# Performance work log

Hardware: AMD Instinct MI355X
Metric: run time of the kernel (lower is better)

Reference implementation:

```python
import jax, jax.numpy as jnp
import numpy as np

B, T, C = 4, 2048, 768
H, D = 6, 128


def apply_rotary_emb(x, cos, sin):
    # x: (B, T, H, D); cos, sin: (1, T, 1, D//2)
    d = x.shape[-1] // 2
    x1, x2 = x[..., :d], x[..., d:]
    y1 = x1 * cos + x2 * sin
    y2 = -x1 * sin + x2 * cos
    return jnp.concatenate([y1, y2], axis=-1)


def rmsnorm(x):
    eps = 1e-15
    ms = jnp.mean(x * x, axis=-1, keepdims=True)
    return x / jnp.sqrt(ms + eps)


def setup_inputs() -> dict:
    key = jax.random.key(0)
    ks = jax.random.split(key, 7)
    s = 0.02
    return {
        "x": jax.random.normal(ks[0], (B, T, C), jnp.float32),
        "cos": jax.random.normal(ks[1], (1, T, 1, D // 2), jnp.float32),
        "sin": jax.random.normal(ks[2], (1, T, 1, D // 2), jnp.float32),
        "Wq": jax.random.normal(ks[3], (C, C), jnp.float32) * s,
        "Wk": jax.random.normal(ks[4], (C, C), jnp.float32) * s,
        "Wv": jax.random.normal(ks[5], (C, C), jnp.float32) * s,
        "Wo": jax.random.normal(ks[6], (C, C), jnp.float32) * s,
    }


def reference(x, cos, sin, Wq, Wk, Wv, Wo):
    b, t, c = x.shape
    # QKV projections (nn.Linear: x @ W.T)
    q = (x @ Wq.T).reshape(b, t, H, D)
    k = (x @ Wk.T).reshape(b, t, H, D)
    v = (x @ Wv.T).reshape(b, t, H, D)
    # RoPE then QK-RMSNorm
    q = rmsnorm(apply_rotary_emb(q, cos, sin))
    k = rmsnorm(apply_rotary_emb(k, cos, sin))
    # (B, H, T, D)
    q = q.transpose(0, 2, 1, 3)
    k = k.transpose(0, 2, 1, 3)
    v = v.transpose(0, 2, 1, 3)
    scores = jnp.einsum('bhqd,bhkd->bhqk', q, k) / jnp.sqrt(jnp.float32(D))
    causal = jnp.tril(jnp.ones((t, t), dtype=bool))
    scores = jnp.where(causal[None, None], scores, -jnp.inf)
    attn = jax.nn.softmax(scores, axis=-1)
    out = jnp.einsum('bhqk,bhkd->bhqd', attn, v)
    out = out.transpose(0, 2, 1, 3).reshape(b, t, c)
    return out @ Wo.T
```

## Files before the change

### kernel.cpp

```cpp
#include <hip/hip_runtime.h>

#define T_SEQ 2048
#define NH    6
#define HD    128
#define CDIM  768
#define NQKV  2304
#define MROWS 8192
#define NSLOT 1104
#define QSCL  0.12754011021989615f

typedef __attribute__((ext_vector_type(8)))  short bf16x8;
typedef __attribute__((ext_vector_type(4)))  float f32x4;
typedef __attribute__((ext_vector_type(16))) float f32x16;
typedef __attribute__((ext_vector_type(2)))  int   i32x2;

__device__ __forceinline__ unsigned short f2bf(float f){
  unsigned int u = __builtin_bit_cast(unsigned int, f);
  u += 0x7fffu + ((u >> 16) & 1u);
  return (unsigned short)(u >> 16);
}
__device__ __forceinline__ float bf2f(unsigned short h){
  unsigned int u = ((unsigned int)h) << 16;
  return __builtin_bit_cast(float, u);
}
__device__ __forceinline__ float ex2(float x){
  return __builtin_amdgcn_exp2f(x);
}
__device__ __forceinline__ unsigned int cvtpk(float lo, float hi){
  unsigned int r;
  asm("v_cvt_pk_bf16_f32 %0, %1, %2" : "=v"(r) : "v"(lo), "v"(hi));
  return r;
}

__device__ __forceinline__ void gload_lds16(const void* g, void* l){
  __builtin_amdgcn_global_load_lds(
      (const __attribute__((address_space(1))) unsigned int*)g,
      (__attribute__((address_space(3))) unsigned int*)l, 16, 0, 0);
}

__device__ __forceinline__ int ncq(int Q){
  return Q < 3 ? 1 : Q < 7 ? 2 : Q < 10 ? 3 : Q < 14 ? 4 : 5;
}
__device__ __forceinline__ int cumc(int Q){
  return Q < 4 ? Q : Q < 8 ? 3 + 2*(Q-3) : Q < 11 ? 11 + 3*(Q-7)
       : Q < 15 ? 20 + 4*(Q-10) : 36 + 5*(Q-14);
}

__global__ __launch_bounds__(256) void cvt_f32_bf16(
    const float* __restrict__ in, unsigned short* __restrict__ out, int n4){
  int i = blockIdx.x * 256 + threadIdx.x;
  if (i >= n4) return;
  float4 v = reinterpret_cast<const float4*>(in)[i];
  ushort4 o;
  o.x = f2bf(v.x); o.y = f2bf(v.y); o.z = f2bf(v.z); o.w = f2bf(v.w);
  reinterpret_cast<ushort4*>(out)[i] = o;
}

__global__ __launch_bounds__(256) void cvt_w4(
    const float* __restrict__ w0, const float* __restrict__ w1,
    const float* __restrict__ w2, const float* __restrict__ w3,
    unsigned short* __restrict__ out){
  const int which = blockIdx.y;
  const float* src = which == 0 ? w0 : which == 1 ? w1 : which == 2 ? w2 : w3;
  int i = blockIdx.x * 256 + threadIdx.x;
  float4 v = reinterpret_cast<const float4*>(src)[i];
  ushort4 o;
  o.x = f2bf(v.x); o.y = f2bf(v.y); o.z = f2bf(v.z); o.w = f2bf(v.w);
  reinterpret_cast<ushort4*>(out + (size_t)which * CDIM * CDIM)[i] = o;
}

template<int EPI>
__global__ __launch_bounds__(256) void gemm_bt(
    const unsigned short* __restrict__ A,
    const unsigned short* __restrict__ B,
    void* __restrict__ Cv, int M, int N, int K,
    const float* __restrict__ cosp, const float* __restrict__ sinp,
    unsigned short* __restrict__ Vt)
{
  __shared__ unsigned short sh[128 * 128];
  unsigned short* As = sh;
  unsigned short* Bs = sh + 128 * 64;
  const int tid  = threadIdx.x;
  const int lane = tid & 63;
  const int wave = tid >> 6;
  const int lr = lane & 15, lg = lane >> 4;
  const int srow = lane >> 3;
  const int sslot = (lane & 7) ^ (lane >> 3);
  const int gx = gridDim.x, gy = gridDim.y, nwg = gx * gy;
  const int flat = blockIdx.y * gx + blockIdx.x;
  const int nf = (flat & 7) * (nwg >> 3) + (flat >> 3);
  const int row0 = (nf / gy) * 128, col0 = (nf % gy) * 128;
  const int wrow = wave * 32;

  f32x4 acc[2][8];
  const f32x4 z = {0.f, 0.f, 0.f, 0.f};
  #pragma unroll
  for (int i = 0; i < 2; ++i)
    #pragma unroll
    for (int j = 0; j < 8; ++j) acc[i][j] = z;

  for (int k0 = 0; k0 < K; k0 += 64){
    #pragma unroll
    for (int i = 0; i < 4; ++i){
      int seg = wave * 4 + i;
      int r = seg * 8 + srow;
      gload_lds16(&A[(size_t)(row0 + r) * K + k0 + sslot * 8], &As[seg * 512]);
      gload_lds16(&B[(size_t)(col0 + r) * K + k0 + sslot * 8], &Bs[seg * 512]);
    }
    __syncthreads();
    #pragma unroll
    for (int kk = 0; kk < 64; kk += 32){
      bf16x8 af[2], bfr[8];
      #pragma unroll
      for (int mi = 0; mi < 2; ++mi)
        af[mi] = *reinterpret_cast<const bf16x8*>(
            &As[(wrow + mi*16 + lr) * 64 + ((((kk>>3) + lg) ^ (lr & 7)) * 8)]);
      #pragma unroll
      for (int ni = 0; ni < 8; ++ni)
        bfr[ni] = *reinterpret_cast<const bf16x8*>(
            &Bs[(ni*16 + lr) * 64 + ((((kk>>3) + lg) ^ (lr & 7)) * 8)]);
      #pragma unroll
      for (int mi = 0; mi < 2; ++mi)
        #pragma unroll
        for (int ni = 0; ni < 8; ++ni)
          acc[mi][ni] = __builtin_amdgcn_mfma_f32_16x16x32_bf16(af[mi], bfr[ni], acc[mi][ni], 0, 0, 0);
    }
    __syncthreads();
  }

  if (EPI == 0){
    float* Cf = reinterpret_cast<float*>(Cv);
    #pragma unroll
    for (int mi = 0; mi < 2; ++mi)
      #pragma unroll
      for (int ni = 0; ni < 8; ++ni)
        #pragma unroll
        for (int r = 0; r < 4; ++r)
          Cf[(size_t)(row0 + wrow + mi*16 + lg*4 + r) * N + col0 + ni*16 + lr] = acc[mi][ni][r];
  } else {
    unsigned short* Cb = reinterpret_cast<unsigned short*>(Cv);
    const int ct = col0 >> 7;
    if (ct >= 12){
      const int hh = ct - 12;
      const int b2 = row0 >> 11, t0 = row0 & (T_SEQ - 1);
      #pragma unroll
      for (int mi = 0; mi < 2; ++mi)
        #pragma unroll
        for (int ni = 0; ni < 8; ++ni)
          #pragma unroll
          for (int r = 0; r < 4; ++r){
            const int trow = wrow + mi*16 + lg*4 + r;
            const int col  = ni*16 + lr;
            sh[trow * 128 + (col ^ ((trow & 7) << 4))] = f2bf(acc[mi][ni][r]);
          }
      __syncthreads();
      const int dd = tid >> 1, tq = (tid & 1) * 64;
      unsigned short* dst =
          Vt + ((size_t)(b2 * NH + hh) * HD + dd) * T_SEQ + t0 + tq;
      #pragma unroll
      for (int j8 = 0; j8 < 8; ++j8){
        union { int4 v; unsigned short u[8]; } w;
        #pragma unroll
        for (int jj = 0; jj < 8; ++jj){
          const int tt = tq + j8 * 8 + jj;
          w.u[jj] = sh[tt * 128 + (dd ^ (jj << 4))];
        }
        *reinterpret_cast<int4*>(&dst[j8 * 8]) = w.v;
      }
    } else {
      const float post = (ct < 6) ? QSCL : 1.0f;
      #pragma unroll
      for (int mi = 0; mi < 2; ++mi){
        #pragma unroll
        for (int r = 0; r < 4; ++r){
          const int row = row0 + wrow + mi*16 + lg*4 + r;
          const int t = row & (T_SEQ - 1);
          float y1[4], y2[4], ssp = 0.f;
          #pragma unroll
          for (int ni = 0; ni < 4; ++ni){
            const int d = ni*16 + lr;
            float c = cosp[t * 64 + d];
            float s = sinp[t * 64 + d];
            float x1 = acc[mi][ni][r], x2 = acc[mi][ni+4][r];
            y1[ni] = x1 * c + x2 * s;
            y2[ni] = x2 * c - x1 * s;
            ssp += y1[ni]*y1[ni] + y2[ni]*y2[ni];
          }
          #pragma unroll
          for (int off = 1; off < 16; off <<= 1) ssp += __shfl_xor(ssp, off);
          const float inv = rsqrtf(ssp * (1.0f / 128.0f) + 1e-15f) * post;
          #pragma unroll
          for (int ni = 0; ni < 4; ++ni){
            const int d = ni*16 + lr;
            Cb[(size_t)row * N + col0 + d]      = f2bf(y1[ni] * inv);
            Cb[(size_t)row * N + col0 + d + 64] = f2bf(y2[ni] * inv);
          }
        }
      }
    }
  }
}

__global__ __launch_bounds__(256) void attn_fwd(
    const unsigned short* __restrict__ QKVb,
    const unsigned short* __restrict__ Vt,
    unsigned short* __restrict__ AO,
    unsigned short* __restrict__ Op, float* __restrict__ Mp, float* __restrict__ Lp)
{
  __shared__ unsigned short Ks[64][136];
  __shared__ unsigned short Vs[128][72];
  const int tid = threadIdx.x;
  const int lane = tid & 63, wave = tid >> 6;
  const int l31 = lane & 31, hi = lane >> 5;

  const int flat = blockIdx.x;
  const int nf = (flat & 7) * 138 + (flat >> 3);
  const int bh = nf / 46;
  const int L = 45 - (nf % 46);
  int Q, c;
  if (L < 3)      { Q = L; c = 0; }
  else if (L < 11){ int m = L - 3;  Q = 3 + (m >> 1);  c = m & 1; }
  else if (L < 20){ int m = L - 11; Q = 7 + m / 3;     c = m % 3; }
  else if (L < 36){ int m = L - 20; Q = 10 + (m >> 2); c = m & 3; }
  else            { int m = L - 36; Q = 14 + m / 5;    c = m % 5; }
  const int nc = ncq(Q);
  const int tiles = 2 * Q + 2;
  const int base = tiles / nc, rem = tiles % nc;
  const int tbeg = c * base + (c < rem ? c : rem);
  const int tend = tbeg + base + (c < rem ? 1 : 0);
  const int b = bh / NH, h = bh % NH;
  const int qw = Q * 128 + wave * 32;

  const unsigned short* Qp = QKVb + (size_t)(b * T_SEQ) * NQKV + h * HD;
  const unsigned short* Kp = QKVb + (size_t)(b * T_SEQ) * NQKV + CDIM + h * HD;
  const unsigned short* Vp = Vt + (size_t)bh * HD * T_SEQ;

  const int kr = tid >> 4, kc4 = (tid & 15) * 8;
  const int vr = tid >> 3, vc4 = (tid & 7) * 8;

  bf16x8 qf[8];
  #pragma unroll
  for (int c4 = 0; c4 < 8; ++c4)
    qf[c4] = *reinterpret_cast<const bf16x8*>(
        &Qp[(size_t)(qw + l31) * NQKV + c4 * 16 + hi * 8]);

  f32x16 o[4];
  #pragma unroll
  for (int db = 0; db < 4; ++db)
    #pragma unroll
    for (int r = 0; r < 16; ++r) o[db][r] = 0.f;
  float mrun = -__builtin_inff(), lrun = 0.f;

  int4 gk0, gk1, gk2, gk3, gv0, gv1, gv2, gv3;
  {
    const int kv0 = tbeg * 64;
    gk0 = *reinterpret_cast<const int4*>(&Kp[(size_t)(kv0 + kr)       * NQKV + kc4]);
    gk1 = *reinterpret_cast<const int4*>(&Kp[(size_t)(kv0 + kr + 16)  * NQKV + kc4]);
    gk2 = *reinterpret_cast<const int4*>(&Kp[(size_t)(kv0 + kr + 32)  * NQKV + kc4]);
    gk3 = *reinterpret_cast<const int4*>(&Kp[(size_t)(kv0 + kr + 48)  * NQKV + kc4]);
    gv0 = *reinterpret_cast<const int4*>(&Vp[(size_t)(vr)       * T_SEQ + kv0 + vc4]);
    gv1 = *reinterpret_cast<const int4*>(&Vp[(size_t)(vr + 32)  * T_SEQ + kv0 + vc4]);
    gv2 = *reinterpret_cast<const int4*>(&Vp[(size_t)(vr + 64)  * T_SEQ + kv0 + vc4]);
    gv3 = *reinterpret_cast<const int4*>(&Vp[(size_t)(vr + 96)  * T_SEQ + kv0 + vc4]);
  }

  for (int t = tbeg; t < tend; ++t){
    *reinterpret_cast<int4*>(&Ks[kr][kc4])        = gk0;
    *reinterpret_cast<int4*>(&Ks[kr + 16][kc4])   = gk1;
    *reinterpret_cast<int4*>(&Ks[kr + 32][kc4])   = gk2;
    *reinterpret_cast<int4*>(&Ks[kr + 48][kc4])   = gk3;
    *reinterpret_cast<int4*>(&Vs[vr][vc4])        = gv0;
    *reinterpret_cast<int4*>(&Vs[vr + 32][vc4])   = gv1;
    *reinterpret_cast<int4*>(&Vs[vr + 64][vc4])   = gv2;
    *reinterpret_cast<int4*>(&Vs[vr + 96][vc4])   = gv3;
    __syncthreads();

    if (t + 1 < tend){
      const int kn = (t + 1) * 64;
      gk0 = *reinterpret_cast<const int4*>(&Kp[(size_t)(kn + kr)       * NQKV + kc4]);
      gk1 = *reinterpret_cast<const int4*>(&Kp[(size_t)(kn + kr + 16)  * NQKV + kc4]);
      gk2 = *reinterpret_cast<const int4*>(&Kp[(size_t)(kn + kr + 32)  * NQKV + kc4]);
      gk3 = *reinterpret_cast<const int4*>(&Kp[(size_t)(kn + kr + 48)  * NQKV + kc4]);
      gv0 = *reinterpret_cast<const int4*>(&Vp[(size_t)(vr)       * T_SEQ + kn + vc4]);
      gv1 = *reinterpret_cast<const int4*>(&Vp[(size_t)(vr + 32)  * T_SEQ + kn + vc4]);
      gv2 = *reinterpret_cast<const int4*>(&Vp[(size_t)(vr + 64)  * T_SEQ + kn + vc4]);
      gv3 = *reinterpret_cast<const int4*>(&Vp[(size_t)(vr + 96)  * T_SEQ + kn + vc4]);
    }

    const int kv0 = t * 64;
    if (kv0 <= qw + 31){
      f32x16 s[2];
      #pragma unroll
      for (int r = 0; r < 16; ++r){ s[0][r] = 0.f; s[1][r] = 0.f; }
      __builtin_amdgcn_s_setprio(1);
      #pragma unroll
      for (int c4 = 0; c4 < 8; ++c4){
        bf16x8 k0 = *reinterpret_cast<const bf16x8*>(&Ks[l31][c4 * 16 + hi * 8]);
        bf16x8 k1 = *reinterpret_cast<const bf16x8*>(&Ks[32 + l31][c4 * 16 + hi * 8]);
        s[0] = __builtin_amdgcn_mfma_f32_32x32x16_bf16(k0, qf[c4], s[0], 0, 0, 0);
        s[1] = __builtin_amdgcn_mfma_f32_32x32x16_bf16(k1, qf[c4], s[1], 0, 0, 0);
      }
      __builtin_amdgcn_s_setprio(0);

      const int qg = qw + l31;
      if (kv0 + 63 > qw){
        #pragma unroll
        for (int blk = 0; blk < 2; ++blk)
          #pragma unroll
          for (int r = 0; r < 16; ++r){
            int kg = kv0 + 32 * blk + (r & 3) + 8 * (r >> 2) + 4 * hi;
            s[blk][r] = (kg <= qg) ? s[blk][r] : -__builtin_inff();
          }
      }

      float t8[8];
      #pragma unroll
      for (int blk = 0; blk < 2; ++blk)
        #pragma unroll
        for (int j = 0; j < 4; ++j)
          t8[blk * 4 + j] = fmaxf(fmaxf(s[blk][4*j], s[blk][4*j+1]),
                                  fmaxf(s[blk][4*j+2], s[blk][4*j+3]));
      float pm = fmaxf(fmaxf(fmaxf(t8[0], t8[1]), fmaxf(t8[2], t8[3])),
                       fmaxf(fmaxf(t8[4], t8[5]), fmaxf(t8[6], t8[7])));
      pm = fmaxf(pm, __shfl_xor(pm, 32));

      if (__any(pm > mrun)){
        float mn = fmaxf(mrun, pm);
        float scf = (mrun == -__builtin_inff()) ? 0.f : ex2(mrun - mn);
        mrun = mn; lrun *= scf;
        #pragma unroll
        for (int r = 0; r < 16; ++r){
          float scr = __shfl(scf, (r & 3) + 8 * (r >> 2) + 4 * hi, 32);
          #pragma unroll
          for (int db = 0; db < 4; ++db) o[db][r] *= scr;
        }
      }

      float a8[8];
      #pragma unroll
      for (int blk = 0; blk < 2; ++blk)
        #pragma unroll
        for (int j = 0; j < 4; ++j){
          float p0 = ex2(s[blk][4*j]   - mrun);
          float p1 = ex2(s[blk][4*j+1] - mrun);
          float p2 = ex2(s[blk][4*j+2] - mrun);
          float p3 = ex2(s[blk][4*j+3] - mrun);
          s[blk][4*j] = p0; s[blk][4*j+1] = p1; s[blk][4*j+2] = p2; s[blk][4*j+3] = p3;
          a8[blk * 4 + j] = (p0 + p1) + (p2 + p3);
        }
      float ls = ((a8[0] + a8[1]) + (a8[2] + a8[3])) + ((a8[4] + a8[5]) + (a8[6] + a8[7]));
      lrun += ls + __shfl_xor(ls, 32);

      __builtin_amdgcn_s_setprio(1);
      #pragma unroll
      for (int kc = 0; kc < 4; ++kc){
        const int blk = kc >> 1, base2 = (kc & 1) * 8;
        unsigned int a0 = cvtpk(s[blk][base2+0], s[blk][base2+1]);
        unsigned int b0 = cvtpk(s[blk][base2+4], s[blk][base2+5]);
        unsigned int a1 = cvtpk(s[blk][base2+2], s[blk][base2+3]);
        unsigned int b1 = cvtpk(s[blk][base2+6], s[blk][base2+7]);
        i32x2 sw0 = __builtin_amdgcn_permlane32_swap((int)a0, (int)b0, false, false);
        i32x2 sw1 = __builtin_amdgcn_permlane32_swap((int)a1, (int)b1, false, false);
        union { bf16x8 v; unsigned int u[4]; } pa;
        pa.u[0] = (unsigned int)sw0[0];
        pa.u[1] = (unsigned int)sw1[0];
        pa.u[2] = (unsigned int)sw0[1];
        pa.u[3] = (unsigned int)sw1[1];
        #pragma unroll
        for (int db = 0; db < 4; ++db){
          bf16x8 vf = *reinterpret_cast<const bf16x8*>(
              &Vs[db * 32 + l31][kc * 16 + hi * 8]);
          o[db] = __builtin_amdgcn_mfma_f32_32x32x16_bf16(pa.v, vf, o[db], 0, 0, 0);
        }
      }
      __builtin_amdgcn_s_setprio(0);
    }
    __syncthreads();
  }

  if (nc == 1){
    float inv = 1.0f / lrun;
    #pragma unroll
    for (int r = 0; r < 16; ++r){
      const int crow = (r & 3) + 8 * (r >> 2) + 4 * hi;
      float ir = __shfl(inv, crow, 32);
      #pragma unroll
      for (int db = 0; db < 4; ++db)
        AO[((size_t)b * T_SEQ + qw + crow) * CDIM + h * HD + db * 32 + l31] =
            f2bf(o[db][r] * ir);
    }
  } else {
    const int slot = bh * 46 + cumc(Q) + c;
    unsigned short* OpW = Op + (size_t)slot * 128 * 128;
    #pragma unroll
    for (int r = 0; r < 16; ++r){
      const int row = wave * 32 + (r & 3) + 8 * (r >> 2) + 4 * hi;
      #pragma unroll
      for (int db = 0; db < 4; ++db)
        OpW[row * 128 + db * 32 + l31] = f2bf(o[db][r]);
    }
    if (hi == 0){
      Mp[(size_t)slot * 128 + wave * 32 + l31] = mrun;
      Lp[(size_t)slot * 128 + wave * 32 + l31] = lrun;
    }
  }
}

__global__ __launch_bounds__(256) void attn_combine(
    const unsigned short* __restrict__ Op, const float* __restrict__ Mp,
    const float* __restrict__ Lp, unsigned short* __restrict__ AO)
{
  const int Q  = 3 + blockIdx.x;
  const int bh = blockIdx.y;
  const int b = bh / NH, h = bh % NH;
  const int nc = ncq(Q);
  const int slot0 = bh * 46 + cumc(Q);
  #pragma unroll
  for (int u = 0; u < 16; ++u){
    int unit = threadIdx.x + u * 256;
    int r = unit >> 5, d4 = unit & 31;
    float m = -__builtin_inff();
    for (int cc = 0; cc < nc; ++cc)
      m = fmaxf(m, Mp[(size_t)(slot0 + cc) * 128 + r]);
    float l = 0.f;
    float a0 = 0.f, a1 = 0.f, a2 = 0.f, a3 = 0.f;
    for (int cc = 0; cc < nc; ++cc){
      float w = __builtin_amdgcn_exp2f(Mp[(size_t)(slot0 + cc) * 128 + r] - m);
      l += w * Lp[(size_t)(slot0 + cc) * 128 + r];
      const ushort4 v = *reinterpret_cast<const ushort4*>(
          &Op[((size_t)(slot0 + cc) * 128 + r) * 128 + d4 * 4]);
      a0 += w * bf2f(v.x); a1 += w * bf2f(v.y);
      a2 += w * bf2f(v.z); a3 += w * bf2f(v.w);
    }
    float inv = 1.0f / l;
    ushort4 ov;
    ov.x = f2bf(a0 * inv); ov.y = f2bf(a1 * inv);
    ov.z = f2bf(a2 * inv); ov.w = f2bf(a3 * inv);
    *reinterpret_cast<ushort4*>(
        &AO[((size_t)b * T_SEQ + Q * 128 + r) * CDIM + h * HD + d4 * 4]) = ov;
  }
}

extern "C" void kernel_launch(void* const* d_in, const int* in_sizes, int n_in,
                              void* d_out, int out_size, void* d_ws, size_t ws_size,
                              hipStream_t stream)
{
  (void)in_sizes; (void)n_in; (void)out_size; (void)ws_size;
  const float* x    = (const float*)d_in[0];
  const float* cosp = (const float*)d_in[1];
  const float* sinp = (const float*)d_in[2];
  const float* Wq   = (const float*)d_in[3];
  const float* Wk   = (const float*)d_in[4];
  const float* Wv   = (const float*)d_in[5];
  const float* Wo   = (const float*)d_in[6];
  float* out = (float*)d_out;

  unsigned short* xb    = (unsigned short*)d_ws;
  unsigned short* Wqkvb = xb    + (size_t)MROWS * CDIM;
  unsigned short* Wob   = Wqkvb + (size_t)NQKV * CDIM;
  unsigned short* QKVb  = Wob   + (size_t)CDIM * CDIM;
  unsigned short* Vtb   = QKVb  + (size_t)MROWS * NQKV;
  unsigned short* AO    = Vtb   + (size_t)MROWS * CDIM;
  unsigned short* Op    = AO    + (size_t)MROWS * CDIM;
  float* Mp = (float*)(Op + (size_t)NSLOT * 128 * 128);
  float* Lp = Mp + (size_t)NSLOT * 128;

  int n4x = MROWS * CDIM / 4;
  cvt_f32_bf16<<<(n4x + 255) / 256, 256, 0, stream>>>(x, xb, n4x);
  cvt_w4<<<dim3(CDIM * CDIM / 4 / 256, 4), 256, 0, stream>>>(Wq, Wk, Wv, Wo, Wqkvb);

  gemm_bt<1><<<dim3(MROWS / 128, NQKV / 128), 256, 0, stream>>>(
      xb, Wqkvb, QKVb, MROWS, NQKV, CDIM, cosp, sinp, Vtb);
  attn_fwd<<<NSLOT, 256, 0, stream>>>(QKVb, Vtb, AO, Op, Mp, Lp);
  attn_combine<<<dim3(13, 24), 256, 0, stream>>>(Op, Mp, Lp, AO);
  gemm_bt<0><<<dim3(MROWS / 128, CDIM / 128), 256, 0, stream>>>(
      AO, Wob, out, MROWS, CDIM, CDIM, nullptr, nullptr, nullptr);
}
```

Baseline: 210.2 us.

## Load K/V tiles directly to LDS with XOR swizzle instead of register staging

Replaces the register-staged K/V prefetch (global loads held in registers across the loop, then written to padded LDS) with direct global-to-LDS 16-byte loads (gload_lds16) into unpadded, XOR-swizzled LDS layouts. Fragment reads apply the same swizzle to avoid bank conflicts, and launch bounds request 4 blocks per SM. This removes the register pressure and LDS write instructions of the staging path, but also drops the software prefetch overlap, so each tile's load latency is now exposed before the barrier unless occupancy hides it.

```diff
diff --git a/kernel.cpp b/kernel.cpp
--- a/kernel.cpp
+++ b/kernel.cpp
@@ -201,14 +201,14 @@
   }
 }
 
-__global__ __launch_bounds__(256) void attn_fwd(
+__global__ __launch_bounds__(256, 4) void attn_fwd(
     const unsigned short* __restrict__ QKVb,
     const unsigned short* __restrict__ Vt,
     unsigned short* __restrict__ AO,
     unsigned short* __restrict__ Op, float* __restrict__ Mp, float* __restrict__ Lp)
 {
-  __shared__ unsigned short Ks[64][136];
-  __shared__ unsigned short Vs[128][72];
+  __shared__ unsigned short Ks[64 * 128];
+  __shared__ unsigned short Vs[128 * 64];
   const int tid = threadIdx.x;
   const int lane = tid & 63, wave = tid >> 6;
   const int l31 = lane & 31, hi = lane >> 5;
@@ -235,8 +235,10 @@
   const unsigned short* Kp = QKVb + (size_t)(b * T_SEQ) * NQKV + CDIM + h * HD;
   const unsigned short* Vp = Vt + (size_t)bh * HD * T_SEQ;
 
-  const int kr = tid >> 4, kc4 = (tid & 15) * 8;
-  const int vr = tid >> 3, vc4 = (tid & 7) * 8;
+  const int krow_in = lane >> 4;
+  const int kslot   = lane & 15;
+  const int vrow_in = lane >> 3;
+  const int vslot   = lane & 7;
 
   bf16x8 qf[8];
   #pragma unroll
@@ -251,43 +253,21 @@
     for (int r = 0; r < 16; ++r) o[db][r] = 0.f;
   float mrun = -__builtin_inff(), lrun = 0.f;
 
-  int4 gk0, gk1, gk2, gk3, gv0, gv1, gv2, gv3;
-  {
-    const int kv0 = tbeg * 64;
-    gk0 = *reinterpret_cast<const int4*>(&Kp[(size_t)(kv0 + kr)       * NQKV + kc4]);
-    gk1 = *reinterpret_cast<const int4*>(&Kp[(size_t)(kv0 + kr + 16)  * NQKV + kc4]);
-    gk2 = *reinterpret_cast<const int4*>(&Kp[(size_t)(kv0 + kr + 32)  * NQKV + kc4]);
-    gk3 = *reinterpret_cast<const int4*>(&Kp[(size_t)(kv0 + kr + 48)  * NQKV + kc4]);
-    gv0 = *reinterpret_cast<const int4*>(&Vp[(size_t)(vr)       * T_SEQ + kv0 + vc4]);
-    gv1 = *reinterpret_cast<const int4*>(&Vp[(size_t)(vr + 32)  * T_SEQ + kv0 + vc4]);
-    gv2 = *reinterpret_cast<const int4*>(&Vp[(size_t)(vr + 64)  * T_SEQ + kv0 + vc4]);
-    gv3 = *reinterpret_cast<const int4*>(&Vp[(size_t)(vr + 96)  * T_SEQ + kv0 + vc4]);
-  }
-
   for (int t = tbeg; t < tend; ++t){
-    *reinterpret_cast<int4*>(&Ks[kr][kc4])        = gk0;
-    *reinterpret_cast<int4*>(&Ks[kr + 16][kc4])   = gk1;
-    *reinterpret_cast<int4*>(&Ks[kr + 32][kc4])   = gk2;
-    *reinterpret_cast<int4*>(&Ks[kr + 48][kc4])   = gk3;
-    *reinterpret_cast<int4*>(&Vs[vr][vc4])        = gv0;
-    *reinterpret_cast<int4*>(&Vs[vr + 32][vc4])   = gv1;
-    *reinterpret_cast<int4*>(&Vs[vr + 64][vc4])   = gv2;
-    *reinterpret_cast<int4*>(&Vs[vr + 96][vc4])   = gv3;
+    const int kv0 = t * 64;
+    #pragma unroll
+    for (int i = 0; i < 4; ++i){
+      const int kseg = wave * 4 + i;
+      const int krow = kseg * 4 + krow_in;
+      const int kgs  = kslot ^ (krow & 7);
+      gload_lds16(Kp + (size_t)(kv0 + krow) * NQKV + kgs * 8, &Ks[kseg * 512]);
+      const int vseg = wave * 4 + i;
+      const int vrow = vseg * 8 + vrow_in;
+      const int vgs  = vslot ^ (vrow & 7);
+      gload_lds16(Vp + (size_t)vrow * T_SEQ + kv0 + vgs * 8, &Vs[vseg * 512]);
+    }
     __syncthreads();
 
-    if (t + 1 < tend){
-      const int kn = (t + 1) * 64;
-      gk0 = *reinterpret_cast<const int4*>(&Kp[(size_t)(kn + kr)       * NQKV + kc4]);
-      gk1 = *reinterpret_cast<const int4*>(&Kp[(size_t)(kn + kr + 16)  * NQKV + kc4]);
-      gk2 = *reinterpret_cast<const int4*>(&Kp[(size_t)(kn + kr + 32)  * NQKV + kc4]);
-      gk3 = *reinterpret_cast<const int4*>(&Kp[(size_t)(kn + kr + 48)  * NQKV + kc4]);
-      gv0 = *reinterpret_cast<const int4*>(&Vp[(size_t)(vr)       * T_SEQ + kn + vc4]);
-      gv1 = *reinterpret_cast<const int4*>(&Vp[(size_t)(vr + 32)  * T_SEQ + kn + vc4]);
-      gv2 = *reinterpret_cast<const int4*>(&Vp[(size_t)(vr + 64)  * T_SEQ + kn + vc4]);
-      gv3 = *reinterpret_cast<const int4*>(&Vp[(size_t)(vr + 96)  * T_SEQ + kn + vc4]);
-    }
-
-    const int kv0 = t * 64;
     if (kv0 <= qw + 31){
       f32x16 s[2];
       #pragma unroll
@@ -295,8 +275,9 @@
       __builtin_amdgcn_s_setprio(1);
       #pragma unroll
       for (int c4 = 0; c4 < 8; ++c4){
-        bf16x8 k0 = *reinterpret_cast<const bf16x8*>(&Ks[l31][c4 * 16 + hi * 8]);
-        bf16x8 k1 = *reinterpret_cast<const bf16x8*>(&Ks[32 + l31][c4 * 16 + hi * 8]);
+        const int ksl = (c4 * 2 + hi) ^ (l31 & 7);
+        bf16x8 k0 = *reinterpret_cast<const bf16x8*>(&Ks[(l31) * 128 + ksl * 8]);
+        bf16x8 k1 = *reinterpret_cast<const bf16x8*>(&Ks[(32 + l31) * 128 + ksl * 8]);
         s[0] = __builtin_amdgcn_mfma_f32_32x32x16_bf16(k0, qf[c4], s[0], 0, 0, 0);
         s[1] = __builtin_amdgcn_mfma_f32_32x32x16_bf16(k1, qf[c4], s[1], 0, 0, 0);
       }
@@ -368,8 +349,9 @@
         pa.u[3] = (unsigned int)sw1[1];
         #pragma unroll
         for (int db = 0; db < 4; ++db){
-          bf16x8 vf = *reinterpret_cast<const bf16x8*>(
-              &Vs[db * 32 + l31][kc * 16 + hi * 8]);
+          const int vrow = db * 32 + l31;
+          const int vsl  = (kc * 2 + hi) ^ (vrow & 7);
+          bf16x8 vf = *reinterpret_cast<const bf16x8*>(&Vs[vrow * 64 + vsl * 8]);
           o[db] = __builtin_amdgcn_mfma_f32_32x32x16_bf16(pa.v, vf, o[db], 0, 0, 0);
         }
       }
```

Result: slower. 362.6 us (+72.5%).
